# Performance work log

Hardware: AMD Instinct MI355X
Metric: run time of the kernel (lower is better)

## Reference

```python
import jax, jax.numpy as jnp
import numpy as np

MAX_WAVELENGTH = 10000.0
BIG_NEG = -2.3819763e+38
NUM_KV_HEADS = 8
HEAD_DIM = 128


def _apply_rope(x, positions):
    # x: [B, L, H, D], positions: [B, L]
    d = x.shape[-1]
    freq_exponents = (2.0 / d) * jnp.arange(d // 2, dtype=jnp.float32)
    timescale = MAX_WAVELENGTH ** freq_exponents                      # [D/2]
    radians = positions.astype(jnp.float32)[..., None] / timescale    # [B, L, D/2]
    radians = radians[..., None, :]                                   # [B, L, 1, D/2]
    sin, cos = jnp.sin(radians), jnp.cos(radians)
    x1, x2 = jnp.split(x, 2, axis=-1)
    return jnp.concatenate([x1 * cos - x2 * sin, x2 * cos + x1 * sin], axis=-1)


def setup_inputs() -> dict:
    key = jax.random.key(0)
    ks = jax.random.split(key, 4)
    B, T, D = 2, 2048, 4096
    N, K, H = 32, NUM_KV_HEADS, HEAD_DIM
    x = jax.random.normal(ks[0], (B, T, D), dtype=jnp.float32)
    positions = jnp.broadcast_to(jnp.arange(T, dtype=jnp.int32), (B, T))
    # causal mask [B, 1, T, S]
    attn_mask = jnp.broadcast_to(jnp.tril(jnp.ones((T, T), dtype=bool))[None, None], (B, 1, T, T))
    scale = 1.0 / np.sqrt(D)
    wq = jax.random.normal(ks[1], (N, D, H), dtype=jnp.float32) * scale
    wkv = jax.random.normal(ks[2], (2, K, D, H), dtype=jnp.float32) * scale
    wo = jax.random.normal(ks[3], (N, H, D), dtype=jnp.float32) * (1.0 / np.sqrt(N * H))
    return {"x": x, "positions": positions, "attn_mask": attn_mask,
            "wq": wq, "wkv": wkv, "wo": wo, "decode": 0}


def reference(x, positions, attn_mask, wq, wkv, wo, decode):
    # decode=False (prefill); KV cache path not exercised.
    B, T, D = x.shape
    N, _, H = wq.shape
    K = wkv.shape[1]
    G = N // K

    q = jnp.einsum('BTD,NDH->BTNH', x, wq)        # [B, T, N, H]
    k, v = jnp.einsum('BSD,2KDH->2BSKH', x, wkv)  # each [B, S, K, H]

    q = _apply_rope(q, positions) * (H ** -0.5)
    k = _apply_rope(k, positions)

    q = q.reshape(B, T, K, G, H)                  # 'B T (K G) H -> B T K G H'
    logits = jnp.einsum('BTKGH,BSKH->BKGTS', q, k).astype(jnp.float32)
    masked = jnp.where(attn_mask[:, :, None, :, :], logits, BIG_NEG)
    probs = jax.nn.softmax(masked, axis=-1).astype(k.dtype)
    encoded = jnp.einsum('BKGTS,BSKH->BTKGH', probs, v)
    encoded = encoded.reshape(B, T, N, H)
    return jnp.einsum('BTNH,NHD->BTD', encoded, wo)
```

## Files before the change

kernel.cpp:

```cpp
#include <hip/hip_runtime.h>

typedef short short8  __attribute__((ext_vector_type(8)));
typedef short short4v __attribute__((ext_vector_type(4)));
typedef float f32x4   __attribute__((ext_vector_type(4)));

#define B_   2
#define T_   2048
#define D_   4096
#define N_   32
#define KH_  8
#define H_   128
#define BT_  (B_*T_)
#define NH_  (N_*H_)

__device__ __forceinline__ short f2bf(float f) {
    unsigned u = __float_as_uint(f);
    u += 0x7fffu + ((u >> 16) & 1u);
    return (short)(u >> 16);
}

__device__ __forceinline__ void gl_lds16(const short* g, short* l) {
    __builtin_amdgcn_global_load_lds(
        (const __attribute__((address_space(1))) void*)(g),
        (__attribute__((address_space(3))) void*)(l), 16, 0, 0);
}

__global__ __launch_bounds__(256) void cast_x_kernel(const float* __restrict__ in,
                                                     short* __restrict__ out) {
    const size_t i = ((size_t)blockIdx.x * 256 + threadIdx.x) * 8;
    float4 v0 = *reinterpret_cast<const float4*>(in + i);
    float4 v1 = *reinterpret_cast<const float4*>(in + i + 4);
    short8 s;
    s[0] = f2bf(v0.x); s[1] = f2bf(v0.y); s[2] = f2bf(v0.z); s[3] = f2bf(v0.w);
    s[4] = f2bf(v1.x); s[5] = f2bf(v1.y); s[6] = f2bf(v1.z); s[7] = f2bf(v1.w);
    *reinterpret_cast<short8*>(out + i) = s;
}

__global__ void transpose_cast_kernel(const float* __restrict__ in,
                                      short* __restrict__ out, int R, int C) {
    __shared__ float tile[32][33];
    const long long slice = blockIdx.z;
    in  += slice * (long long)R * C;
    out += slice * (long long)R * C;
    const int c0 = blockIdx.x * 32, r0 = blockIdx.y * 32;
    const int tx = threadIdx.x, ty = threadIdx.y;
#pragma unroll
    for (int i = 0; i < 4; i++) {
        int r = r0 + ty + i * 8;
        tile[ty + i * 8][tx] = in[(long long)r * C + c0 + tx];
    }
    __syncthreads();
#pragma unroll
    for (int i = 0; i < 4; i++) {
        int cc = c0 + ty + i * 8;
        out[(long long)cc * R + r0 + tx] = f2bf(tile[tx][ty + i * 8]);
    }
}

__global__ __launch_bounds__(256) void qkv_gemm_kernel(
    const short* __restrict__ xb, const int* __restrict__ positions,
    const short* __restrict__ wqt, const short* __restrict__ wkvt,
    short* __restrict__ qo, short* __restrict__ ko, short* __restrict__ vto)
{
    __shared__ short As[128 * 32];
    __shared__ short Bs[128 * 32];
    const int hb  = blockIdx.x;
    const int m0  = blockIdx.y * 128;
    const int tid = threadIdx.x;
    const int w = tid >> 6, lane = tid & 63;
    const int quad = lane >> 4, l15 = lane & 15;
    const int arow = lane >> 2, aslot = lane & 3;

    const short* Bbase = (hb < 32) ? (wqt + (size_t)hb * H_ * D_)
                                   : (wkvt + (size_t)(hb - 32) * H_ * D_);

    f32x4 acc[2][8];
    const f32x4 zero4 = {0.f, 0.f, 0.f, 0.f};
#pragma unroll
    for (int jr = 0; jr < 2; jr++)
#pragma unroll
        for (int jc = 0; jc < 8; jc++) acc[jr][jc] = zero4;

    for (int kt = 0; kt < D_ / 32; kt++) {
        const int kk0 = kt * 32;
        __syncthreads();
#pragma unroll
        for (int i = 0; i < 2; i++) {
            const int ci = 2 * w + i;
            const int row = ci * 16 + arow;
            const int sl = aslot ^ (row & 3);
            gl_lds16(xb + (size_t)(m0 + row) * D_ + kk0 + sl * 8, &As[ci * 512]);
            gl_lds16(Bbase + (size_t)row * D_ + kk0 + sl * 8, &Bs[ci * 512]);
        }
        __syncthreads();
        short8 a[2], bq[8];
        const int fs = (quad ^ (l15 & 3)) * 8;
#pragma unroll
        for (int jr = 0; jr < 2; jr++)
            a[jr] = *reinterpret_cast<const short8*>(&As[(32 * w + 16 * jr + l15) * 32 + fs]);
#pragma unroll
        for (int jc = 0; jc < 8; jc++)
            bq[jc] = *reinterpret_cast<const short8*>(&Bs[(16 * jc + l15) * 32 + fs]);
#pragma unroll
        for (int jr = 0; jr < 2; jr++)
#pragma unroll
            for (int jc = 0; jc < 8; jc++)
                acc[jr][jc] = __builtin_amdgcn_mfma_f32_16x16x32_bf16(a[jr], bq[jc], acc[jr][jc], 0, 0, 0);
    }

    if (hb < 40) {
        float qs;
        if (hb < 32) { qs = 0.08838834764831845f * 1.4426950408889634f; }
        else         { qs = 1.0f; }
#pragma unroll
        for (int jr = 0; jr < 2; jr++) {
#pragma unroll
            for (int reg = 0; reg < 4; reg++) {
                const int bt = m0 + 32 * w + 16 * jr + quad * 4 + reg;
                const int b = bt >> 11, t = bt & (T_ - 1);
                short* dst = (hb < 32)
                    ? qo + ((size_t)(b * N_ + hb) * T_ + t) * H_
                    : ko + ((size_t)(b * KH_ + (hb - 32)) * T_ + t) * H_;
                const float pos = (float)positions[bt];
#pragma unroll
                for (int jc = 0; jc < 4; jc++) {
                    const int h2 = 16 * jc + l15;
                    float inv_ts = exp2f((float)h2 * -0.20762050593048935f);
                    float rev = pos * inv_ts * 0.15915494309189535f;
                    rev -= floorf(rev);
                    float sn, cs;
                    __sincosf(rev * 6.283185307179586f, &sn, &cs);
                    float x1 = acc[jr][jc][reg], x2 = acc[jr][jc + 4][reg];
                    dst[h2]      = f2bf((x1 * cs - x2 * sn) * qs);
                    dst[h2 + 64] = f2bf((x2 * cs + x1 * sn) * qs);
                }
            }
        }
    } else {
        const int vh = hb - 40;
        const int b = m0 >> 11;
#pragma unroll
        for (int jr = 0; jr < 2; jr++) {
            const int t0r = (m0 - b * T_) + 32 * w + 16 * jr + quad * 4;
#pragma unroll
            for (int jc = 0; jc < 8; jc++) {
                const int h = 16 * jc + l15;
                short4v pv;
                pv[0] = f2bf(acc[jr][jc][0]); pv[1] = f2bf(acc[jr][jc][1]);
                pv[2] = f2bf(acc[jr][jc][2]); pv[3] = f2bf(acc[jr][jc][3]);
                *reinterpret_cast<short4v*>(vto + ((size_t)(b * KH_ + vh) * H_ + h) * T_ + t0r) = pv;
            }
        }
    }
}

__global__ __launch_bounds__(256) void attn_kernel(
    const short* __restrict__ qp, const short* __restrict__ kp,
    const short* __restrict__ vtp, short* __restrict__ encp)
{
    __shared__ short ldsP[4 * 32 * 128];
    const int tid = threadIdx.x;
    const int w = tid >> 6, lane = tid & 63;
    const int quad = lane >> 4, l15 = lane & 15;
    const int widx = blockIdx.x * 4 + w;
    const int pr = widx & 31;
    const int n  = (widx >> 5) & 31;
    const int b  = widx >> 10;
    const int kh = n >> 2;
    short* P = ldsP + w * (32 * 128);

    const short* qbase = qp  + (size_t)(b * N_  + n)  * T_ * H_;
    const short* kbase = kp  + (size_t)(b * KH_ + kh) * T_ * H_;
    const short* vbase = vtp + (size_t)(b * KH_ + kh) * H_ * T_;

    const f32x4 zero4 = {0.f, 0.f, 0.f, 0.f};

    for (int half = 0; half < 2; half++) {
        const int wt = half ? pr : (63 - pr);
        const int t0 = wt * 32;

        short8 qf[2][4];
#pragma unroll
        for (int jc = 0; jc < 2; jc++)
#pragma unroll
            for (int ks = 0; ks < 4; ks++)
                qf[jc][ks] = *reinterpret_cast<const short8*>(
                    qbase + (size_t)(t0 + 16 * jc + l15) * H_ + ks * 32 + quad * 8);

        f32x4 o[2][8];
#pragma unroll
        for (int jm = 0; jm < 2; jm++)
#pragma unroll
            for (int jn = 0; jn < 8; jn++) o[jm][jn] = zero4;
        float lsum[2] = {0.f, 0.f};

        short8 kb[8];
        short8 vb[8];
#pragma unroll
        for (int jn = 0; jn < 8; jn++)
            vb[jn] = *reinterpret_cast<const short8*>(
                vbase + (size_t)(16 * jn + l15) * T_ + quad * 8);
#pragma unroll
        for (int ks = 0; ks < 4; ks++)
#pragma unroll
            for (int jr = 0; jr < 2; jr++)
                kb[2 * ks + jr] = *reinterpret_cast<const short8*>(
                    kbase + (size_t)(16 * jr + l15) * H_ + ks * 32 + quad * 8);

        for (int ss = 0; ss <= wt; ss++) {
            const int s0 = ss * 32;
            const int slot = (ss & 3) * 4;
            const int s0n = (ss < wt) ? s0 + 32 : 0;

            f32x4 s[2][2];
#pragma unroll
            for (int jr = 0; jr < 2; jr++)
#pragma unroll
                for (int jc = 0; jc < 2; jc++) s[jr][jc] = zero4;
#pragma unroll
            for (int ks = 0; ks < 4; ks++)
#pragma unroll
                for (int jr = 0; jr < 2; jr++)
#pragma unroll
                    for (int jc = 0; jc < 2; jc++)
                        s[jr][jc] = __builtin_amdgcn_mfma_f32_16x16x32_bf16(kb[2 * ks + jr], qf[jc][ks], s[jr][jc], 0, 0, 0);

#pragma unroll
            for (int ks = 0; ks < 4; ks++)
#pragma unroll
                for (int jr = 0; jr < 2; jr++)
                    kb[2 * ks + jr] = *reinterpret_cast<const short8*>(
                        kbase + (size_t)(s0n + 16 * jr + l15) * H_ + ks * 32 + quad * 8);

            if (ss == wt) {
#pragma unroll
                for (int jr = 0; jr < 2; jr++)
#pragma unroll
                    for (int jc = 0; jc < 2; jc++)
#pragma unroll
                        for (int reg = 0; reg < 4; reg++) {
                            int sl = 16 * jr + 4 * quad + reg;
                            int tl = 16 * jc + l15;
                            if (sl > tl) s[jr][jc][reg] = -1.0e30f;
                        }
            }

#pragma unroll
            for (int jr = 0; jr < 2; jr++)
#pragma unroll
                for (int jc = 0; jc < 2; jc++) {
                    short4v pk;
#pragma unroll
                    for (int reg = 0; reg < 4; reg++) {
                        float p = exp2f(s[jr][jc][reg]);
                        lsum[jc] += p;
                        pk[reg] = f2bf(p);
                    }
                    const int row = 16 * jc + l15;
                    const int cc  = slot + 2 * jr + (quad >> 1);
                    const int hf  = quad & 1;
                    *reinterpret_cast<short4v*>(
                        &P[row * 128 + ((cc ^ l15) << 3) + (hf << 2)]) = pk;
                }
            asm volatile("s_waitcnt lgkmcnt(0)" ::: "memory");

#pragma unroll
            for (int jm = 0; jm < 2; jm++) {
                short8 pa = *reinterpret_cast<const short8*>(
                    &P[(16 * jm + l15) * 128 + (((slot + quad) ^ l15) << 3)]);
#pragma unroll
                for (int jn = 0; jn < 8; jn++)
                    o[jm][jn] = __builtin_amdgcn_mfma_f32_16x16x32_bf16(pa, vb[jn], o[jm][jn], 0, 0, 0);
            }

#pragma unroll
            for (int jn = 0; jn < 8; jn++)
                vb[jn] = *reinterpret_cast<const short8*>(
                    vbase + (size_t)(16 * jn + l15) * T_ + s0n + quad * 8);
        }

#pragma unroll
        for (int jc = 0; jc < 2; jc++) {
            lsum[jc] += __shfl_xor(lsum[jc], 16, 64);
            lsum[jc] += __shfl_xor(lsum[jc], 32, 64);
        }
#pragma unroll
        for (int jm = 0; jm < 2; jm++)
#pragma unroll
            for (int reg = 0; reg < 4; reg++) {
                const float inv = 1.0f / __shfl(lsum[jm], 4 * quad + reg, 64);
                const int t = t0 + 16 * jm + 4 * quad + reg;
                const size_t base = (size_t)(b * T_ + t) * NH_ + n * H_;
#pragma unroll
                for (int jn = 0; jn < 8; jn++)
                    encp[base + 16 * jn + l15] = f2bf(o[jm][jn][reg] * inv);
            }
    }
}

__global__ __launch_bounds__(256) void out_gemm_kernel(
    const short* __restrict__ enc, const short* __restrict__ wot,
    float* __restrict__ out)
{
    __shared__ short As[128 * 32];
    __shared__ short Bs[128 * 32];
    const int d0 = blockIdx.x * 128;
    const int m0 = blockIdx.y * 128;
    const int tid = threadIdx.x;
    const int w = tid >> 6, lane = tid & 63;
    const int quad = lane >> 4, l15 = lane & 15;
    const int arow = lane >> 2, aslot = lane & 3;

    f32x4 acc[2][8];
    const f32x4 zero4 = {0.f, 0.f, 0.f, 0.f};
#pragma unroll
    for (int jr = 0; jr < 2; jr++)
#pragma unroll
        for (int jc = 0; jc < 8; jc++) acc[jr][jc] = zero4;

    for (int kt = 0; kt < NH_ / 32; kt++) {
        const int kk0 = kt * 32;
        __syncthreads();
#pragma unroll
        for (int i = 0; i < 2; i++) {
            const int ci = 2 * w + i;
            const int row = ci * 16 + arow;
            const int sl = aslot ^ (row & 3);
            gl_lds16(enc + (size_t)(m0 + row) * NH_ + kk0 + sl * 8, &As[ci * 512]);
            gl_lds16(wot + (size_t)(d0 + row) * NH_ + kk0 + sl * 8, &Bs[ci * 512]);
        }
        __syncthreads();
        short8 a[2], bq[8];
        const int fs = (quad ^ (l15 & 3)) * 8;
#pragma unroll
        for (int jr = 0; jr < 2; jr++)
            a[jr] = *reinterpret_cast<const short8*>(&As[(32 * w + 16 * jr + l15) * 32 + fs]);
#pragma unroll
        for (int jc = 0; jc < 8; jc++)
            bq[jc] = *reinterpret_cast<const short8*>(&Bs[(16 * jc + l15) * 32 + fs]);
#pragma unroll
        for (int jr = 0; jr < 2; jr++)
#pragma unroll
            for (int jc = 0; jc < 8; jc++)
                acc[jr][jc] = __builtin_amdgcn_mfma_f32_16x16x32_bf16(a[jr], bq[jc], acc[jr][jc], 0, 0, 0);
    }

#pragma unroll
    for (int jr = 0; jr < 2; jr++)
#pragma unroll
        for (int jc = 0; jc < 8; jc++)
#pragma unroll
            for (int reg = 0; reg < 4; reg++) {
                int r = m0 + 32 * w + 16 * jr + quad * 4 + reg;
                out[(size_t)r * D_ + d0 + 16 * jc + l15] = acc[jr][jc][reg];
            }
}

extern "C" void kernel_launch(void* const* d_in, const int* in_sizes, int n_in,
                              void* d_out, int out_size, void* d_ws, size_t ws_size,
                              hipStream_t stream)
{
    const float* x         = (const float*)d_in[0];
    const int*   positions = (const int*)d_in[1];
    const float* wq        = (const float*)d_in[3];
    const float* wkv       = (const float*)d_in[4];
    const float* wo        = (const float*)d_in[5];
    float* out = (float*)d_out;

    char* ws = (char*)d_ws;
    short* wqt  = (short*)(ws);
    short* wkvt = (short*)(ws + 33554432);
    short* q    = (short*)(ws + 50331648);
    short* kx   = (short*)(ws + 83886080);
    short* vt   = (short*)(ws + 92274688);
    short* xbf  = (short*)(ws + 100663296);
    short* wot  = (short*)(ws + 100663296);
    short* enc  = (short*)(ws);

    dim3 tb(32, 8);
    cast_x_kernel<<<dim3((BT_ * (size_t)D_) / 2048), dim3(256), 0, stream>>>(x, xbf);
    transpose_cast_kernel<<<dim3(H_/32, D_/32, N_),    tb, 0, stream>>>(wq,  wqt,  D_,  H_);
    transpose_cast_kernel<<<dim3(H_/32, D_/32, 2*KH_), tb, 0, stream>>>(wkv, wkvt, D_,  H_);

    qkv_gemm_kernel<<<dim3(48, BT_/128), dim3(256), 0, stream>>>(xbf, positions, wqt, wkvt, q, kx, vt);

    transpose_cast_kernel<<<dim3(D_/32, NH_/32, 1),    tb, 0, stream>>>(wo,  wot,  NH_, D_);

    attn_kernel<<<dim3(512), dim3(256), 0, stream>>>(q, kx, vt, enc);
    out_gemm_kernel<<<dim3(D_/128, BT_/128), dim3(256), 0, stream>>>(enc, wot, out);
}
```

Before: 925.5 us.

## Replace QKV and output GEMMs with 256x256 double-buffered 8-wave pipelined kernel

Both projection GEMMs move from a 128x128 tile with a 32-wide K step and a full sync per step to a shared macro. The new kernel uses 512 threads, a 256x256 tile, a 64-wide K step and double-buffered LDS filled by global_load_lds. Loads for the next K tile are interleaved between four MFMA quarter-phases, with vmcnt waits, s_barrier and s_setprio. The aim is to hide global load latency and raise the ratio of MFMA work to LDS traffic. The QKV kernel now relies on wkvt sitting directly after wqt in the workspace, so heads 32-47 index past wqt, and it uses more LDS and registers per block.

```diff
diff --git a/kernel.cpp b/kernel.cpp
--- a/kernel.cpp
+++ b/kernel.cpp
@@ -12,6 +12,7 @@
 #define H_   128
 #define BT_  (B_*T_)
 #define NH_  (N_*H_)
+#define NTK  64
 
 __device__ __forceinline__ short f2bf(float f) {
     unsigned u = __float_as_uint(f);
@@ -57,101 +58,174 @@
     }
 }
 
-__global__ __launch_bounds__(256) void qkv_gemm_kernel(
+
+#define RD_A(cb, jm) {                                                          \
+    const int rr_ = arow0 + (jm) * 16;                                          \
+    a[jm][0] = *reinterpret_cast<const short8*>(&lds[cb][0][ah][rr_ * 64 + at0]); \
+    a[jm][1] = *reinterpret_cast<const short8*>(&lds[cb][0][ah][rr_ * 64 + at1]); }
+
+#define RD_B(cb, jn, jj) {                                                      \
+    const int rb_ = (jn) * 16 + l15;                                            \
+    b[jj][0] = *reinterpret_cast<const short8*>(&lds[cb][1][wc][rb_ * 64 + at0]); \
+    b[jj][1] = *reinterpret_cast<const short8*>(&lds[cb][1][wc][rb_ * 64 + at1]); }
+
+#define STAGE(ab, G, rowbase, sb, h, kt_) {                                     \
+    int kt_c = (kt_); if (kt_c > NTK - 1) kt_c = NTK - 1;                       \
+    const short* gsrc_ = (G) + (size_t)((rowbase) + (h) * 128 + srow) * 4096    \
+                             + kt_c * 64 + sca * 8;                             \
+    gl_lds16(gsrc_,            &lds[sb][ab][h][(2 * w) * 512]);                 \
+    gl_lds16(gsrc_ + 8 * 4096, &lds[sb][ab][h][(2 * w) * 512 + 512]); }
+
+#define MFMA_Q(JM0, JN0)                                                        \
+    __builtin_amdgcn_s_setprio(1);                                              \
+    _Pragma("unroll")                                                           \
+    for (int jm_ = 0; jm_ < 2; ++jm_)                                           \
+    _Pragma("unroll")                                                           \
+    for (int jn_ = 0; jn_ < 4; ++jn_)                                           \
+    _Pragma("unroll")                                                           \
+    for (int ks_ = 0; ks_ < 2; ++ks_)                                           \
+        acc[(JM0) + jm_][(JN0) + jn_] = __builtin_amdgcn_mfma_f32_16x16x32_bf16( \
+            a[(JM0) + jm_][ks_], b[jn_][ks_], acc[(JM0) + jm_][(JN0) + jn_], 0, 0, 0); \
+    __builtin_amdgcn_s_setprio(0);
+
+#define GEMM8_PRO_AND_LOOP(Ap, Bp, m0, n0)                                      \
+    f32x4 acc[4][8];                                                            \
+    {const f32x4 z_ = {0.f,0.f,0.f,0.f};                                        \
+    _Pragma("unroll") for (int jm_=0;jm_<4;++jm_)                               \
+    _Pragma("unroll") for (int jn_=0;jn_<8;++jn_) acc[jm_][jn_]=z_;}            \
+    short8 a[4][2], b[4][2];                                                    \
+    STAGE(0, Ap, m0, 0, 0, 0); STAGE(0, Ap, m0, 0, 1, 0);                       \
+    STAGE(1, Bp, n0, 0, 0, 0); STAGE(1, Bp, n0, 0, 1, 0);                       \
+    STAGE(0, Ap, m0, 1, 0, 1); STAGE(0, Ap, m0, 1, 1, 1);                       \
+    for (int i = 0; i < NTK / 2; ++i) {                                         \
+        _Pragma("unroll")                                                       \
+        for (int hf = 0; hf < 2; ++hf) {                                        \
+            const int cb = hf, sbB = hf ^ 1;                                    \
+            const int tB = 2 * i + 1 + hf;                                      \
+            const int tA = 2 * i + 2 + hf;                                      \
+                                                                        \
+            asm volatile("s_waitcnt vmcnt(4)" ::: "memory");                    \
+            __builtin_amdgcn_s_barrier();                                       \
+            RD_A(cb, 0); RD_A(cb, 1);                                           \
+            RD_B(cb, 0, 0); RD_B(cb, 1, 1); RD_B(cb, 2, 2); RD_B(cb, 3, 3);     \
+            STAGE(1, Bp, n0, sbB, 0, tB);                                       \
+            MFMA_Q(0, 0);                                                       \
+                                                                        \
+            __builtin_amdgcn_s_barrier();                                       \
+            RD_A(cb, 2); RD_A(cb, 3);                                           \
+            STAGE(1, Bp, n0, sbB, 1, tB);                                       \
+            MFMA_Q(2, 0);                                                       \
+                                                                        \
+            __builtin_amdgcn_s_barrier();                                       \
+            RD_B(cb, 4, 0); RD_B(cb, 5, 1); RD_B(cb, 6, 2); RD_B(cb, 7, 3);     \
+            STAGE(0, Ap, m0, hf, 0, tA);                                        \
+            MFMA_Q(2, 4);                                                       \
+                                                                        \
+            __builtin_amdgcn_s_barrier();                                       \
+            STAGE(0, Ap, m0, hf, 1, tA);                                        \
+            MFMA_Q(0, 4);                                                       \
+        }                                                                       \
+    }                                                                           \
+    asm volatile("s_waitcnt vmcnt(0)" ::: "memory");
+
+__global__ __launch_bounds__(512, 2) void qkv_gemm8_kernel(
     const short* __restrict__ xb, const int* __restrict__ positions,
-    const short* __restrict__ wqt, const short* __restrict__ wkvt,
+    const short* __restrict__ wqt,
     short* __restrict__ qo, short* __restrict__ ko, short* __restrict__ vto)
 {
-    __shared__ short As[128 * 32];
-    __shared__ short Bs[128 * 32];
-    const int hb  = blockIdx.x;
-    const int m0  = blockIdx.y * 128;
+    __shared__ short lds[2][2][2][8192];
     const int tid = threadIdx.x;
     const int w = tid >> 6, lane = tid & 63;
     const int quad = lane >> 4, l15 = lane & 15;
-    const int arow = lane >> 2, aslot = lane & 3;
-
-    const short* Bbase = (hb < 32) ? (wqt + (size_t)hb * H_ * D_)
-                                   : (wkvt + (size_t)(hb - 32) * H_ * D_);
-
-    f32x4 acc[2][8];
-    const f32x4 zero4 = {0.f, 0.f, 0.f, 0.f};
-#pragma unroll
-    for (int jr = 0; jr < 2; jr++)
-#pragma unroll
-        for (int jc = 0; jc < 8; jc++) acc[jr][jc] = zero4;
-
-    for (int kt = 0; kt < D_ / 32; kt++) {
-        const int kk0 = kt * 32;
-        __syncthreads();
-#pragma unroll
-        for (int i = 0; i < 2; i++) {
-            const int ci = 2 * w + i;
-            const int row = ci * 16 + arow;
-            const int sl = aslot ^ (row & 3);
-            gl_lds16(xb + (size_t)(m0 + row) * D_ + kk0 + sl * 8, &As[ci * 512]);
-            gl_lds16(Bbase + (size_t)row * D_ + kk0 + sl * 8, &Bs[ci * 512]);
-        }
-        __syncthreads();
-        short8 a[2], bq[8];
-        const int fs = (quad ^ (l15 & 3)) * 8;
-#pragma unroll
-        for (int jr = 0; jr < 2; jr++)
-            a[jr] = *reinterpret_cast<const short8*>(&As[(32 * w + 16 * jr + l15) * 32 + fs]);
-#pragma unroll
-        for (int jc = 0; jc < 8; jc++)
-            bq[jc] = *reinterpret_cast<const short8*>(&Bs[(16 * jc + l15) * 32 + fs]);
-#pragma unroll
-        for (int jr = 0; jr < 2; jr++)
-#pragma unroll
-            for (int jc = 0; jc < 8; jc++)
-                acc[jr][jc] = __builtin_amdgcn_mfma_f32_16x16x32_bf16(a[jr], bq[jc], acc[jr][jc], 0, 0, 0);
-    }
-
-    if (hb < 40) {
-        float qs;
-        if (hb < 32) { qs = 0.08838834764831845f * 1.4426950408889634f; }
-        else         { qs = 1.0f; }
-#pragma unroll
-        for (int jr = 0; jr < 2; jr++) {
-#pragma unroll
-            for (int reg = 0; reg < 4; reg++) {
-                const int bt = m0 + 32 * w + 16 * jr + quad * 4 + reg;
-                const int b = bt >> 11, t = bt & (T_ - 1);
-                short* dst = (hb < 32)
-                    ? qo + ((size_t)(b * N_ + hb) * T_ + t) * H_
-                    : ko + ((size_t)(b * KH_ + (hb - 32)) * T_ + t) * H_;
+    const int wr = w >> 1, wc = w & 1;
+    const int ah = wr >> 1;
+    const int arow0 = (wr & 1) * 64 + l15;
+    const int sw = l15 & 7;
+    const int at0 = (quad ^ sw) * 8;
+    const int at1 = ((4 + quad) ^ sw) * 8;
+    const int srow = 16 * w + (lane >> 3);
+    const int sca = (lane & 7) ^ (lane >> 3);
+    const int m0 = blockIdx.y * 256;
+    const int n0 = blockIdx.x * 256;
+
+    GEMM8_PRO_AND_LOOP(xb, wqt, m0, n0)
+
+    const int head = 2 * blockIdx.x + wc;
+    if (head < 40) {
+        const float qs = (head < 32) ? (0.08838834764831845f * 1.4426950408889634f) : 1.0f;
+#pragma unroll
+        for (int jm = 0; jm < 4; ++jm) {
+#pragma unroll
+            for (int reg = 0; reg < 4; ++reg) {
+                const int bt = m0 + wr * 64 + jm * 16 + quad * 4 + reg;
+                const int bb = bt >> 11, t = bt & (T_ - 1);
+                short* dst = (head < 32)
+                    ? qo + ((size_t)(bb * N_ + head) * T_ + t) * H_
+                    : ko + ((size_t)(bb * KH_ + (head - 32)) * T_ + t) * H_;
                 const float pos = (float)positions[bt];
 #pragma unroll
-                for (int jc = 0; jc < 4; jc++) {
-                    const int h2 = 16 * jc + l15;
+                for (int jn = 0; jn < 4; ++jn) {
+                    const int h2 = jn * 16 + l15;
                     float inv_ts = exp2f((float)h2 * -0.20762050593048935f);
                     float rev = pos * inv_ts * 0.15915494309189535f;
                     rev -= floorf(rev);
                     float sn, cs;
                     __sincosf(rev * 6.283185307179586f, &sn, &cs);
-                    float x1 = acc[jr][jc][reg], x2 = acc[jr][jc + 4][reg];
+                    float x1 = acc[jm][jn][reg], x2 = acc[jm][jn + 4][reg];
                     dst[h2]      = f2bf((x1 * cs - x2 * sn) * qs);
                     dst[h2 + 64] = f2bf((x2 * cs + x1 * sn) * qs);
                 }
             }
         }
     } else {
-        const int vh = hb - 40;
-        const int b = m0 >> 11;
-#pragma unroll
-        for (int jr = 0; jr < 2; jr++) {
-            const int t0r = (m0 - b * T_) + 32 * w + 16 * jr + quad * 4;
-#pragma unroll
-            for (int jc = 0; jc < 8; jc++) {
-                const int h = 16 * jc + l15;
+        const int vh = head - 40;
+        const int bb = m0 >> 11;
+        const int tl0 = (m0 & (T_ - 1)) + wr * 64;
+#pragma unroll
+        for (int jm = 0; jm < 4; ++jm) {
+            const int t0r = tl0 + jm * 16 + quad * 4;
+#pragma unroll
+            for (int jn = 0; jn < 8; ++jn) {
+                const int h = jn * 16 + l15;
                 short4v pv;
-                pv[0] = f2bf(acc[jr][jc][0]); pv[1] = f2bf(acc[jr][jc][1]);
-                pv[2] = f2bf(acc[jr][jc][2]); pv[3] = f2bf(acc[jr][jc][3]);
-                *reinterpret_cast<short4v*>(vto + ((size_t)(b * KH_ + vh) * H_ + h) * T_ + t0r) = pv;
+                pv[0] = f2bf(acc[jm][jn][0]); pv[1] = f2bf(acc[jm][jn][1]);
+                pv[2] = f2bf(acc[jm][jn][2]); pv[3] = f2bf(acc[jm][jn][3]);
+                *reinterpret_cast<short4v*>(vto + ((size_t)(bb * KH_ + vh) * H_ + h) * T_ + t0r) = pv;
             }
         }
     }
+}
+
+__global__ __launch_bounds__(512, 2) void out_gemm8_kernel(
+    const short* __restrict__ enc, const short* __restrict__ wot,
+    float* __restrict__ out)
+{
+    __shared__ short lds[2][2][2][8192];
+    const int tid = threadIdx.x;
+    const int w = tid >> 6, lane = tid & 63;
+    const int quad = lane >> 4, l15 = lane & 15;
+    const int wr = w >> 1, wc = w & 1;
+    const int ah = wr >> 1;
+    const int arow0 = (wr & 1) * 64 + l15;
+    const int sw = l15 & 7;
+    const int at0 = (quad ^ sw) * 8;
+    const int at1 = ((4 + quad) ^ sw) * 8;
+    const int srow = 16 * w + (lane >> 3);
+    const int sca = (lane & 7) ^ (lane >> 3);
+    const int m0 = blockIdx.y * 256;
+    const int n0 = blockIdx.x * 256;
+
+    GEMM8_PRO_AND_LOOP(enc, wot, m0, n0)
+
+#pragma unroll
+    for (int jm = 0; jm < 4; ++jm)
+#pragma unroll
+        for (int jn = 0; jn < 8; ++jn)
+#pragma unroll
+            for (int reg = 0; reg < 4; ++reg) {
+                const int r = m0 + wr * 64 + jm * 16 + quad * 4 + reg;
+                out[(size_t)r * D_ + n0 + wc * 128 + jn * 16 + l15] = acc[jm][jn][reg];
+            }
 }
 
 __global__ __launch_bounds__(256) void attn_kernel(
@@ -298,64 +372,6 @@
     }
 }
 
-__global__ __launch_bounds__(256) void out_gemm_kernel(
-    const short* __restrict__ enc, const short* __restrict__ wot,
-    float* __restrict__ out)
-{
-    __shared__ short As[128 * 32];
-    __shared__ short Bs[128 * 32];
-    const int d0 = blockIdx.x * 128;
-    const int m0 = blockIdx.y * 128;
-    const int tid = threadIdx.x;
-    const int w = tid >> 6, lane = tid & 63;
-    const int quad = lane >> 4, l15 = lane & 15;
-    const int arow = lane >> 2, aslot = lane & 3;
-
-    f32x4 acc[2][8];
-    const f32x4 zero4 = {0.f, 0.f, 0.f, 0.f};
-#pragma unroll
-    for (int jr = 0; jr < 2; jr++)
-#pragma unroll
-        for (int jc = 0; jc < 8; jc++) acc[jr][jc] = zero4;
-
-    for (int kt = 0; kt < NH_ / 32; kt++) {
-        const int kk0 = kt * 32;
-        __syncthreads();
-#pragma unroll
-        for (int i = 0; i < 2; i++) {
-            const int ci = 2 * w + i;
-            const int row = ci * 16 + arow;
-            const int sl = aslot ^ (row & 3);
-            gl_lds16(enc + (size_t)(m0 + row) * NH_ + kk0 + sl * 8, &As[ci * 512]);
-            gl_lds16(wot + (size_t)(d0 + row) * NH_ + kk0 + sl * 8, &Bs[ci * 512]);
-        }
-        __syncthreads();
-        short8 a[2], bq[8];
-        const int fs = (quad ^ (l15 & 3)) * 8;
-#pragma unroll
-        for (int jr = 0; jr < 2; jr++)
-            a[jr] = *reinterpret_cast<const short8*>(&As[(32 * w + 16 * jr + l15) * 32 + fs]);
-#pragma unroll
-        for (int jc = 0; jc < 8; jc++)
-            bq[jc] = *reinterpret_cast<const short8*>(&Bs[(16 * jc + l15) * 32 + fs]);
-#pragma unroll
-        for (int jr = 0; jr < 2; jr++)
-#pragma unroll
-            for (int jc = 0; jc < 8; jc++)
-                acc[jr][jc] = __builtin_amdgcn_mfma_f32_16x16x32_bf16(a[jr], bq[jc], acc[jr][jc], 0, 0, 0);
-    }
-
-#pragma unroll
-    for (int jr = 0; jr < 2; jr++)
-#pragma unroll
-        for (int jc = 0; jc < 8; jc++)
-#pragma unroll
-            for (int reg = 0; reg < 4; reg++) {
-                int r = m0 + 32 * w + 16 * jr + quad * 4 + reg;
-                out[(size_t)r * D_ + d0 + 16 * jc + l15] = acc[jr][jc][reg];
-            }
-}
-
 extern "C" void kernel_launch(void* const* d_in, const int* in_sizes, int n_in,
                               void* d_out, int out_size, void* d_ws, size_t ws_size,
                               hipStream_t stream)
@@ -382,10 +398,11 @@
     transpose_cast_kernel<<<dim3(H_/32, D_/32, N_),    tb, 0, stream>>>(wq,  wqt,  D_,  H_);
     transpose_cast_kernel<<<dim3(H_/32, D_/32, 2*KH_), tb, 0, stream>>>(wkv, wkvt, D_,  H_);
 
-    qkv_gemm_kernel<<<dim3(48, BT_/128), dim3(256), 0, stream>>>(xbf, positions, wqt, wkvt, q, kx, vt);
+    qkv_gemm8_kernel<<<dim3(24, 16), dim3(512), 0, stream>>>(xbf, positions, wqt, q, kx, vt);
 
     transpose_cast_kernel<<<dim3(D_/32, NH_/32, 1),    tb, 0, stream>>>(wo,  wot,  NH_, D_);
 
     attn_kernel<<<dim3(512), dim3(256), 0, stream>>>(q, kx, vt, enc);
-    out_gemm_kernel<<<dim3(D_/128, BT_/128), dim3(256), 0, stream>>>(enc, wot, out);
-}
+
+    out_gemm8_kernel<<<dim3(16, 16), dim3(512), 0, stream>>>(enc, wot, out);
+}
```

New measurement: 788.7 us. 1.17x faster.
